# Optimization experiments

Hardware: AMD Instinct MI355X
Metric: run time of the kernel (lower is better)

## Reference

```python
import jax, jax.numpy as jnp
import numpy as np

H = 4096      # hidden_size (Llama-7B)
I = 11008     # intermediate_size (Llama-7B)
T = 4096      # tokens = batch 2 * seq 2048


def setup_inputs() -> dict:
    key = jax.random.key(0)
    ks = jax.random.split(key, 10)
    # int8 activations in [-128, 127]
    x = jax.random.randint(ks[0], (T, H), -128, 128, dtype=jnp.int32).astype(jnp.int8)
    # int4 weights stored as int8 values in [-8, 7], layout [out, in]
    gate_w = jax.random.randint(ks[1], (I, H), -8, 8, dtype=jnp.int32).astype(jnp.int8)
    up_w   = jax.random.randint(ks[2], (I, H), -8, 8, dtype=jnp.int32).astype(jnp.int8)
    down_w = jax.random.randint(ks[3], (H, I), -8, 8, dtype=jnp.int32).astype(jnp.int8)
    # per-output-channel dequant scale (input_scale * weight_scale) and fp32 bias
    gate_alpha = jax.random.uniform(ks[4], (I,), jnp.float32, 1e-4, 3e-4)
    up_alpha   = jax.random.uniform(ks[5], (I,), jnp.float32, 1e-4, 3e-4)
    down_alpha = jax.random.uniform(ks[6], (H,), jnp.float32, 1e-4, 3e-4)
    gate_bias = jax.random.normal(ks[7], (I,), jnp.float32) * 0.01
    up_bias   = jax.random.normal(ks[8], (I,), jnp.float32) * 0.01
    down_bias = jax.random.normal(ks[9], (H,), jnp.float32) * 0.01
    down_input_scale = jnp.array(0.1, dtype=jnp.float32)
    return dict(x=x, gate_w=gate_w, up_w=up_w, down_w=down_w,
                gate_alpha=gate_alpha, gate_bias=gate_bias,
                up_alpha=up_alpha, up_bias=up_bias,
                down_alpha=down_alpha, down_bias=down_bias,
                down_input_scale=down_input_scale)


def _w4a8_linear(x_i8, w_i4, alpha, bias):
    # int8 act x int4 weight -> int32 accumulate, per-out-channel dequant, fp32 out
    acc = jnp.matmul(x_i8.astype(jnp.int32), w_i4.T.astype(jnp.int32))  # [T, out]
    return acc.astype(jnp.float32) * alpha + bias


def reference(x, gate_w, up_w, down_w, gate_alpha, gate_bias, up_alpha, up_bias,
              down_alpha, down_bias, down_input_scale):
    g = _w4a8_linear(x, gate_w, gate_alpha, gate_bias)          # [T, I] fp32
    u = _w4a8_linear(x, up_w, up_alpha, up_bias)                # [T, I] fp32
    h = jax.nn.silu(g) * u                                      # SwiGLU
    # requantize to int8 for down_proj input (values kept exact as fp32)
    hq = jnp.clip(jnp.round(h / down_input_scale), -128.0, 127.0)
    out = jnp.matmul(hq, down_w.T.astype(jnp.float32)) * down_alpha + down_bias
    return out
```

## Files before the change

### kernel.cpp

```cpp
#include <hip/hip_runtime.h>
#include <stdint.h>

#define H_DIM 4096
#define I_DIM 11008
#define T_DIM 4096

typedef int i32x4 __attribute__((ext_vector_type(4)));
typedef const void __attribute__((address_space(1))) gvoid_t;
typedef void __attribute__((address_space(3))) svoid_t;

__device__ __forceinline__ void gload_lds16(const void* gsrc, void* ldst) {
    __builtin_amdgcn_global_load_lds((gvoid_t*)gsrc, (svoid_t*)ldst, 16, 0, 0);
}
__device__ __forceinline__ void wait_vmcnt3() {
    asm volatile("s_waitcnt vmcnt(3)" ::: "memory");
}
__device__ __forceinline__ void wait_vmcnt0() {
    asm volatile("s_waitcnt vmcnt(0)" ::: "memory");
}
__device__ __forceinline__ void wait_lgkm0() {
    asm volatile("s_waitcnt lgkmcnt(0)" ::: "memory");
    __builtin_amdgcn_sched_barrier(0);
}
__device__ __forceinline__ void barrier_() {
    asm volatile("s_barrier" ::: "memory");
}

__device__ __forceinline__ uint32_t pack4(int4 v) {
    uint32_t r = (uint32_t)(uint8_t)v.x;
    r |= (uint32_t)(uint8_t)v.y << 8;
    r |= (uint32_t)(uint8_t)v.z << 16;
    r |= (uint32_t)(uint8_t)v.w << 24;
    return r;
}

__global__ void convert_kernel(const int* __restrict__ src, int8_t* __restrict__ dst,
                               int n4) {
    int idx = blockIdx.x * blockDim.x + threadIdx.x;
    int stride = gridDim.x * blockDim.x;
    for (int i = idx; i < n4; i += stride) {
        int4 v = ((const int4*)src)[i];
        ((uint32_t*)dst)[i] = pack4(v);
    }
}

#define MFMA_I8 __builtin_amdgcn_mfma_i32_16x16x64_i8

__global__ __launch_bounds__(512, 4)
void gateup_kernel(const int8_t* __restrict__ x8, const int8_t* __restrict__ gw8,
                   const int8_t* __restrict__ uw8,
                   const float* __restrict__ galpha, const float* __restrict__ gbias,
                   const float* __restrict__ ualpha, const float* __restrict__ ubias,
                   const float* __restrict__ scale_p, int8_t* __restrict__ hq)
{
    __shared__ __align__(16) int8_t smem_s[49152];
    int8_t* lsA = smem_s;
    int8_t* lsG = smem_s + 16384;
    int8_t* lsU = smem_s + 32768;

    const int bid = blockIdx.x;
    const int mt = bid & 31;
    const int nt = bid >> 5;
    const int m0 = mt << 7;
    const int n0 = nt << 7;

    const int tid  = threadIdx.x;
    const int lane = tid & 63;
    const int wid  = tid >> 6;
    const int isU  = wid >> 2;
    const int w4   = wid & 3;
    const int wr   = w4 >> 1;
    const int wc   = w4 & 1;
    const int lr   = lane & 15;
    const int rdsw = ((lane >> 4) ^ ((lr >> 1) & 3)) << 4;

    const int srow = tid >> 2;
    const int scol = ((tid & 3) ^ ((tid >> 3) & 3)) << 4;
    const int woff = wid << 10;

    const int8_t* As = x8  + (size_t)(m0 + srow) * H_DIM + scol;
    const int8_t* Gs = gw8 + (size_t)(n0 + srow) * H_DIM + scol;
    const int8_t* Us = uw8 + (size_t)(n0 + srow) * H_DIM + scol;

    i32x4 acc[4][4];
#pragma unroll
    for (int mf = 0; mf < 4; ++mf)
#pragma unroll
        for (int nf = 0; nf < 4; ++nf) acc[mf][nf] = i32x4{0, 0, 0, 0};

    const int aro = (wr * 64 + lr) * 64 + rdsw;
    const int bro = (wc * 64 + lr) * 64 + rdsw;
    const int8_t* myB = isU ? lsU : lsG;

#define STAGE3(b, kb) do { \
        gload_lds16(As + (kb), lsA + (b) * 8192 + woff); \
        gload_lds16(Gs + (kb), lsG + (b) * 8192 + woff); \
        gload_lds16(Us + (kb), lsU + (b) * 8192 + woff); \
    } while (0)

    const int NKT = H_DIM / 64;
    STAGE3(0, 0);
    STAGE3(1, 64);

    for (int t = 0; t < NKT; ++t) {
        const int cur = t & 1;
        wait_vmcnt3();
        barrier_();
        i32x4 af[4], bf[4];
#pragma unroll
        for (int mf = 0; mf < 4; ++mf)
            af[mf] = *(const i32x4*)(lsA + cur * 8192 + aro + mf * 1024);
#pragma unroll
        for (int nf = 0; nf < 4; ++nf)
            bf[nf] = *(const i32x4*)(myB + cur * 8192 + bro + nf * 1024);
        wait_lgkm0();
        barrier_();
        STAGE3(cur, ((t + 2) & (NKT - 1)) << 6);
#pragma unroll
        for (int mf = 0; mf < 4; ++mf)
#pragma unroll
            for (int nf = 0; nf < 4; ++nf)
                acc[mf][nf] = MFMA_I8(af[mf], bf[nf], acc[mf][nf], 0, 0, 0);
    }
#undef STAGE3
    wait_vmcnt0();
    barrier_();

    const float scale = *scale_p;
#pragma unroll
    for (int h = 0; h < 2; ++h) {
        if (isU) {
#pragma unroll
            for (int mf = 0; mf < 4; ++mf)
#pragma unroll
                for (int q = 0; q < 2; ++q)
                    *(i32x4*)(smem_s + w4 * 8192 + mf * 2048 + q * 1024 + lane * 16)
                        = acc[mf][h * 2 + q];
        }
        barrier_();
        if (!isU) {
#pragma unroll
            for (int q = 0; q < 2; ++q) {
                const int nf = h * 2 + q;
                const int col = n0 + wc * 64 + nf * 16 + lr;
                const float gA = galpha[col], gB = gbias[col];
                const float uA = ualpha[col], uB = ubias[col];
#pragma unroll
                for (int mf = 0; mf < 4; ++mf) {
                    i32x4 uacc = *(const i32x4*)(smem_s + w4 * 8192 + mf * 2048
                                                 + q * 1024 + lane * 16);
                    const int row0 = m0 + wr * 64 + mf * 16 + (lane >> 4) * 4;
#pragma unroll
                    for (int j = 0; j < 4; ++j) {
                        float g = (float)acc[mf][nf][j] * gA + gB;
                        float u = (float)uacc[j] * uA + uB;
                        float s = 1.0f / (1.0f + __expf(-g));
                        float hh = g * s * u;
                        float qv = rintf(hh / scale);
                        qv = fminf(127.0f, fmaxf(-128.0f, qv));
                        hq[(size_t)(row0 + j) * I_DIM + col] = (int8_t)qv;
                    }
                }
            }
        }
        barrier_();
    }
}

__global__ __launch_bounds__(512, 4)
void down_kernel(const int8_t* __restrict__ hq, const int8_t* __restrict__ dw8,
                 const float* __restrict__ dalpha, const float* __restrict__ dbias,
                 float* __restrict__ out)
{
    __shared__ __align__(16) int8_t smem_d[49152];
    int8_t* lsA = smem_d;
    int8_t* lsB = smem_d + 16384;

    const int bid = blockIdx.x;
    const int mt = bid & 31;
    const int nt = bid >> 5;
    const int m0 = mt << 7;
    const int n0 = nt << 8;

    const int tid  = threadIdx.x;
    const int lane = tid & 63;
    const int wid  = tid >> 6;
    const int wr   = wid >> 2;
    const int wc   = wid & 3;
    const int lr   = lane & 15;
    const int rdsw = ((lane >> 4) ^ ((lr >> 1) & 3)) << 4;

    const int srow = tid >> 2;
    const int scol = ((tid & 3) ^ ((tid >> 3) & 3)) << 4;
    const int woff = wid << 10;

    const int8_t* Ap = hq  + (size_t)(m0 + srow) * I_DIM + scol;
    const int8_t* Bp = dw8 + (size_t)(n0 + srow) * I_DIM + scol;

    i32x4 acc[4][4];
#pragma unroll
    for (int mf = 0; mf < 4; ++mf)
#pragma unroll
        for (int nf = 0; nf < 4; ++nf) acc[mf][nf] = i32x4{0, 0, 0, 0};

    const int aro = (wr * 64 + lr) * 64 + rdsw;
    const int bro = (wc * 64 + lr) * 64 + rdsw;

#define STAGE3(b, kb) do { \
        gload_lds16(Ap + (kb), lsA + (b) * 8192 + woff); \
        gload_lds16(Bp + (kb), lsB + (b) * 16384 + woff); \
        gload_lds16(Bp + (kb) + (size_t)128 * I_DIM, lsB + (b) * 16384 + 8192 + woff); \
    } while (0)

    const int NKT = I_DIM / 64;
    STAGE3(0, 0);
    STAGE3(1, 64);

    for (int t = 0; t < NKT; ++t) {
        const int cur = t & 1;
        wait_vmcnt3();
        barrier_();
        i32x4 af[4], bf[4];
#pragma unroll
        for (int mf = 0; mf < 4; ++mf)
            af[mf] = *(const i32x4*)(lsA + cur * 8192 + aro + mf * 1024);
#pragma unroll
        for (int nf = 0; nf < 4; ++nf)
            bf[nf] = *(const i32x4*)(lsB + cur * 16384 + bro + nf * 1024);
        wait_lgkm0();
        barrier_();
        {
            const int t2 = (t + 2 < NKT) ? (t + 2) : (t + 2 - NKT);
            STAGE3(cur, t2 * 64);
        }
#pragma unroll
        for (int mf = 0; mf < 4; ++mf)
#pragma unroll
            for (int nf = 0; nf < 4; ++nf)
                acc[mf][nf] = MFMA_I8(af[mf], bf[nf], acc[mf][nf], 0, 0, 0);
    }
#undef STAGE3
    wait_vmcnt0();

#pragma unroll
    for (int nf = 0; nf < 4; ++nf) {
        const int col = n0 + wc * 64 + nf * 16 + lr;
        const float dA = dalpha[col], dB = dbias[col];
#pragma unroll
        for (int mf = 0; mf < 4; ++mf) {
            const int row0 = m0 + wr * 64 + mf * 16 + (lane >> 4) * 4;
#pragma unroll
            for (int j = 0; j < 4; ++j) {
                out[(size_t)(row0 + j) * H_DIM + col] = (float)acc[mf][nf][j] * dA + dB;
            }
        }
    }
}

extern "C" void kernel_launch(void* const* d_in, const int* in_sizes, int n_in,
                              void* d_out, int out_size, void* d_ws, size_t ws_size,
                              hipStream_t stream) {
    const int* x32  = (const int*)d_in[0];
    const int* gw32 = (const int*)d_in[1];
    const int* uw32 = (const int*)d_in[2];
    const int* dw32 = (const int*)d_in[3];
    const float* ga = (const float*)d_in[4];
    const float* gb = (const float*)d_in[5];
    const float* ua = (const float*)d_in[6];
    const float* ub = (const float*)d_in[7];
    const float* da = (const float*)d_in[8];
    const float* db = (const float*)d_in[9];
    const float* sc = (const float*)d_in[10];
    float* out = (float*)d_out;

    const size_t SZ_X8 = (size_t)T_DIM * H_DIM;
    const size_t SZ_W  = (size_t)I_DIM * H_DIM;
    const size_t SZ_HQ = (size_t)T_DIM * I_DIM;

    int8_t* gw8 = (int8_t*)d_ws;
    int8_t* uw8 = gw8 + SZ_W;
    int8_t* hq  = uw8 + SZ_W;
    int8_t* x8  = hq + SZ_HQ;

    convert_kernel<<<dim3(2048), dim3(256), 0, stream>>>(x32, x8, (int)(SZ_X8 / 4));
    convert_kernel<<<dim3(2048), dim3(256), 0, stream>>>(gw32, gw8, (int)(SZ_W / 4));
    convert_kernel<<<dim3(2048), dim3(256), 0, stream>>>(uw32, uw8, (int)(SZ_W / 4));
    gateup_kernel<<<dim3(32 * 86), dim3(512), 0, stream>>>(
        x8, gw8, uw8, ga, gb, ua, ub, sc, hq);
    int8_t* dw8 = gw8;
    convert_kernel<<<dim3(2048), dim3(256), 0, stream>>>(dw32, dw8, (int)(SZ_W / 4));
    down_kernel<<<dim3(32 * 16), dim3(512), 0, stream>>>(hq, dw8, da, db, out);
}
```

Measured before the change: 715.1 us.

## Load B weight fragments directly from global into registers, skip LDS staging

Both GEMM kernels now fetch the weight (B) operand straight from global memory into registers in MFMA fragment layout, double-buffered across iterations. Only the activation tile A still goes through LDS. This cuts LDS footprint and LDS read traffic for B and may allow higher occupancy. The cost is that weight tiles are no longer shared between waves via LDS, so global/L2 traffic for B rises, and more vector registers are held in flight. The vmcnt wait threshold is adjusted to cover the extra outstanding loads.

Measured after the change: 1.256 ms. 75.6% more time.

```diff
diff --git a/kernel.cpp b/kernel.cpp
--- a/kernel.cpp
+++ b/kernel.cpp
@@ -12,8 +12,8 @@
 __device__ __forceinline__ void gload_lds16(const void* gsrc, void* ldst) {
     __builtin_amdgcn_global_load_lds((gvoid_t*)gsrc, (svoid_t*)ldst, 16, 0, 0);
 }
-__device__ __forceinline__ void wait_vmcnt3() {
-    asm volatile("s_waitcnt vmcnt(3)" ::: "memory");
+__device__ __forceinline__ void wait_vmcnt5() {
+    asm volatile("s_waitcnt vmcnt(5)" ::: "memory");
 }
 __device__ __forceinline__ void wait_vmcnt0() {
     asm volatile("s_waitcnt vmcnt(0)" ::: "memory");
@@ -53,10 +53,8 @@
                    const float* __restrict__ ualpha, const float* __restrict__ ubias,
                    const float* __restrict__ scale_p, int8_t* __restrict__ hq)
 {
-    __shared__ __align__(16) int8_t smem_s[49152];
+    __shared__ __align__(16) int8_t smem_s[32768];
     int8_t* lsA = smem_s;
-    int8_t* lsG = smem_s + 16384;
-    int8_t* lsU = smem_s + 32768;
 
     const int bid = blockIdx.x;
     const int mt = bid & 31;
@@ -78,9 +76,9 @@
     const int scol = ((tid & 3) ^ ((tid >> 3) & 3)) << 4;
     const int woff = wid << 10;
 
-    const int8_t* As = x8  + (size_t)(m0 + srow) * H_DIM + scol;
-    const int8_t* Gs = gw8 + (size_t)(n0 + srow) * H_DIM + scol;
-    const int8_t* Us = uw8 + (size_t)(n0 + srow) * H_DIM + scol;
+    const int8_t* As = x8 + (size_t)(m0 + srow) * H_DIM + scol;
+    const int8_t* Bsel = isU ? uw8 : gw8;
+    const int8_t* Bp = Bsel + (size_t)(n0 + wc * 64 + lr) * H_DIM + ((lane >> 4) << 4);
 
     i32x4 acc[4][4];
 #pragma unroll
@@ -89,40 +87,41 @@
         for (int nf = 0; nf < 4; ++nf) acc[mf][nf] = i32x4{0, 0, 0, 0};
 
     const int aro = (wr * 64 + lr) * 64 + rdsw;
-    const int bro = (wc * 64 + lr) * 64 + rdsw;
-    const int8_t* myB = isU ? lsU : lsG;
-
-#define STAGE3(b, kb) do { \
-        gload_lds16(As + (kb), lsA + (b) * 8192 + woff); \
-        gload_lds16(Gs + (kb), lsG + (b) * 8192 + woff); \
-        gload_lds16(Us + (kb), lsU + (b) * 8192 + woff); \
+
+#define STAGE_A(b, kb) gload_lds16(As + (kb), lsA + (b) * 8192 + woff)
+#define BLOAD(BF, kb) do { \
+        _Pragma("unroll") for (int nf = 0; nf < 4; ++nf) \
+            BF[nf] = *(const i32x4*)(Bp + (size_t)nf * 16 * H_DIM + (kb)); \
+    } while (0)
+
+#define ITER_GU(tt, BF, BFN) do { \
+        wait_vmcnt5(); \
+        barrier_(); \
+        i32x4 af[4]; \
+        _Pragma("unroll") for (int mf = 0; mf < 4; ++mf) \
+            af[mf] = *(const i32x4*)(lsA + ((tt) & 1) * 8192 + aro + mf * 1024); \
+        wait_lgkm0(); \
+        barrier_(); \
+        BLOAD(BFN, (((tt) + 1) & (NKT - 1)) << 6); \
+        STAGE_A((tt) & 1, (((tt) + 2) & (NKT - 1)) << 6); \
+        _Pragma("unroll") for (int mf = 0; mf < 4; ++mf) \
+        _Pragma("unroll") for (int nf = 0; nf < 4; ++nf) \
+            acc[mf][nf] = MFMA_I8(af[mf], BF[nf], acc[mf][nf], 0, 0, 0); \
     } while (0)
 
     const int NKT = H_DIM / 64;
-    STAGE3(0, 0);
-    STAGE3(1, 64);
-
-    for (int t = 0; t < NKT; ++t) {
-        const int cur = t & 1;
-        wait_vmcnt3();
-        barrier_();
-        i32x4 af[4], bf[4];
-#pragma unroll
-        for (int mf = 0; mf < 4; ++mf)
-            af[mf] = *(const i32x4*)(lsA + cur * 8192 + aro + mf * 1024);
-#pragma unroll
-        for (int nf = 0; nf < 4; ++nf)
-            bf[nf] = *(const i32x4*)(myB + cur * 8192 + bro + nf * 1024);
-        wait_lgkm0();
-        barrier_();
-        STAGE3(cur, ((t + 2) & (NKT - 1)) << 6);
-#pragma unroll
-        for (int mf = 0; mf < 4; ++mf)
-#pragma unroll
-            for (int nf = 0; nf < 4; ++nf)
-                acc[mf][nf] = MFMA_I8(af[mf], bf[nf], acc[mf][nf], 0, 0, 0);
-    }
-#undef STAGE3
+    i32x4 bfA[4], bfB[4];
+    STAGE_A(0, 0);
+    BLOAD(bfA, 0);
+    STAGE_A(1, 64);
+
+    for (int t = 0; t < NKT; t += 2) {
+        ITER_GU(t, bfA, bfB);
+        ITER_GU(t + 1, bfB, bfA);
+    }
+#undef ITER_GU
+#undef BLOAD
+#undef STAGE_A
     wait_vmcnt0();
     barrier_();
 
@@ -172,9 +171,8 @@
                  const float* __restrict__ dalpha, const float* __restrict__ dbias,
                  float* __restrict__ out)
 {
-    __shared__ __align__(16) int8_t smem_d[49152];
+    __shared__ __align__(16) int8_t smem_d[16384];
     int8_t* lsA = smem_d;
-    int8_t* lsB = smem_d + 16384;
 
     const int bid = blockIdx.x;
     const int mt = bid & 31;
@@ -194,8 +192,8 @@
     const int scol = ((tid & 3) ^ ((tid >> 3) & 3)) << 4;
     const int woff = wid << 10;
 
-    const int8_t* Ap = hq  + (size_t)(m0 + srow) * I_DIM + scol;
-    const int8_t* Bp = dw8 + (size_t)(n0 + srow) * I_DIM + scol;
+    const int8_t* Ap = hq + (size_t)(m0 + srow) * I_DIM + scol;
+    const int8_t* Bp = dw8 + (size_t)(n0 + wc * 64 + lr) * I_DIM + ((lane >> 4) << 4);
 
     i32x4 acc[4][4];
 #pragma unroll
@@ -204,42 +202,41 @@
         for (int nf = 0; nf < 4; ++nf) acc[mf][nf] = i32x4{0, 0, 0, 0};
 
     const int aro = (wr * 64 + lr) * 64 + rdsw;
-    const int bro = (wc * 64 + lr) * 64 + rdsw;
-
-#define STAGE3(b, kb) do { \
-        gload_lds16(Ap + (kb), lsA + (b) * 8192 + woff); \
-        gload_lds16(Bp + (kb), lsB + (b) * 16384 + woff); \
-        gload_lds16(Bp + (kb) + (size_t)128 * I_DIM, lsB + (b) * 16384 + 8192 + woff); \
+
+#define STAGE_A(b, kb) gload_lds16(Ap + (kb), lsA + (b) * 8192 + woff)
+#define BLOAD(BF, kb) do { \
+        _Pragma("unroll") for (int nf = 0; nf < 4; ++nf) \
+            BF[nf] = *(const i32x4*)(Bp + (size_t)nf * 16 * I_DIM + (kb)); \
+    } while (0)
+
+#define ITER_D(tt, BF, BFN) do { \
+        wait_vmcnt5(); \
+        barrier_(); \
+        i32x4 af[4]; \
+        _Pragma("unroll") for (int mf = 0; mf < 4; ++mf) \
+            af[mf] = *(const i32x4*)(lsA + ((tt) & 1) * 8192 + aro + mf * 1024); \
+        wait_lgkm0(); \
+        barrier_(); \
+        BLOAD(BFN, (size_t)((((tt) + 1) % NKT) * 64)); \
+        STAGE_A((tt) & 1, (((tt) + 2) % NKT) * 64); \
+        _Pragma("unroll") for (int mf = 0; mf < 4; ++mf) \
+        _Pragma("unroll") for (int nf = 0; nf < 4; ++nf) \
+            acc[mf][nf] = MFMA_I8(af[mf], BF[nf], acc[mf][nf], 0, 0, 0); \
     } while (0)
 
     const int NKT = I_DIM / 64;
-    STAGE3(0, 0);
-    STAGE3(1, 64);
-
-    for (int t = 0; t < NKT; ++t) {
-        const int cur = t & 1;
-        wait_vmcnt3();
-        barrier_();
-        i32x4 af[4], bf[4];
-#pragma unroll
-        for (int mf = 0; mf < 4; ++mf)
-            af[mf] = *(const i32x4*)(lsA + cur * 8192 + aro + mf * 1024);
-#pragma unroll
-        for (int nf = 0; nf < 4; ++nf)
-            bf[nf] = *(const i32x4*)(lsB + cur * 16384 + bro + nf * 1024);
-        wait_lgkm0();
-        barrier_();
-        {
-            const int t2 = (t + 2 < NKT) ? (t + 2) : (t + 2 - NKT);
-            STAGE3(cur, t2 * 64);
-        }
-#pragma unroll
-        for (int mf = 0; mf < 4; ++mf)
-#pragma unroll
-            for (int nf = 0; nf < 4; ++nf)
-                acc[mf][nf] = MFMA_I8(af[mf], bf[nf], acc[mf][nf], 0, 0, 0);
-    }
-#undef STAGE3
+    i32x4 bfA[4], bfB[4];
+    STAGE_A(0, 0);
+    BLOAD(bfA, 0);
+    STAGE_A(1, 64);
+
+    for (int t = 0; t < NKT; t += 2) {
+        ITER_D(t, bfA, bfB);
+        ITER_D(t + 1, bfB, bfA);
+    }
+#undef ITER_D
+#undef BLOAD
+#undef STAGE_A
     wait_vmcnt0();
 
 #pragma unroll
```
